# Kernel optimization log

Measured on AMD Instinct MI355X. Metric: run time of the kernel, lower is better.

## Reference

```python
import jax, jax.numpy as jnp
import numpy as np

B, L, D = 16, 1024, 768   # batch, nodes per graph, embed_dim
H, C = 4, 256             # gat_heads, gat_hidden per head
E = 8192                  # directed edges per graph (2 per triple)
NEG_SLOPE = 0.2           # PyG GATConv default negative_slope


def setup_inputs() -> dict:
    key = jax.random.key(0)
    ks = jax.random.split(key, 8)
    s = 0.02
    return {
        "text_embeddings": jax.random.normal(ks[0], (B, L, D), jnp.float32),
        "edge_index": jax.random.randint(ks[1], (B, 2, E), 0, L, jnp.int32),
        "W_gat": jax.random.normal(ks[2], (H * C, D), jnp.float32) * s,   # GATConv.lin (bias=False)
        "att_src": jax.random.normal(ks[3], (H, C), jnp.float32) * s,
        "att_dst": jax.random.normal(ks[4], (H, C), jnp.float32) * s,
        "b_gat": jnp.zeros((H * C,), jnp.float32),                        # GATConv bias (concat=True)
        "W_out": jax.random.normal(ks[5], (D, H * C + D), jnp.float32) * s,
        "b_out": jnp.zeros((D,), jnp.float32),
    }


def _gat_one(x, edge_index, W_gat, att_src, att_dst, b_gat):
    """PyG-style GATConv on one graph. x: [N,D], edge_index: [2,E] (src->dst)."""
    N = x.shape[0]
    loops = jnp.arange(N, dtype=edge_index.dtype)          # add_self_loops=True (PyG default)
    src = jnp.concatenate([edge_index[0], loops])
    dst = jnp.concatenate([edge_index[1], loops])
    h = (x @ W_gat.T).reshape(N, H, C)                     # [N,H,C]
    a_s = jnp.einsum('nhc,hc->nh', h, att_src)             # [N,H]
    a_d = jnp.einsum('nhc,hc->nh', h, att_dst)
    e = jax.nn.leaky_relu(a_s[src] + a_d[dst], NEG_SLOPE)  # [E+N,H] per-edge logits
    m = jax.ops.segment_max(e, dst, num_segments=N)        # stable softmax over each dst neighborhood
    p = jnp.exp(e - m[dst])
    denom = jax.ops.segment_sum(p, dst, num_segments=N)
    alpha = p / (denom[dst] + 1e-16)                       # [E+N,H]
    out = jax.ops.segment_sum(alpha[:, :, None] * h[src], dst, num_segments=N)  # [N,H,C]
    return out.reshape(N, H * C) + b_gat


def reference(text_embeddings, edge_index, W_gat, att_src, att_dst, b_gat, W_out, b_out):
    x_gat = jax.vmap(_gat_one, in_axes=(0, 0, None, None, None, None))(
        text_embeddings, edge_index, W_gat, att_src, att_dst, b_gat)   # [B,L,H*C]
    fused = jnp.concatenate([text_embeddings, x_gat], axis=-1)          # [B,L,D+H*C]
    return fused @ W_out.T + b_out                                      # [B,L,D]
```

## Files before the change

kernel.cpp:

```cpp
#include <hip/hip_runtime.h>
#include <hip/hip_bf16.h>

#define B_ 16
#define L_ 1024
#define D_ 768
#define H_ 4
#define C_ 256
#define E_ 8192
#define ET_ (E_ + L_)
#define HC_ (H_ * C_)
#define F_ (D_ + HC_)
#define M_ (B_ * L_)
#define NEG_SLOPE 0.2f

typedef short bf16x8 __attribute__((ext_vector_type(8)));
typedef float f32x16 __attribute__((ext_vector_type(16)));
using bf16 = __hip_bfloat16;

struct bf16x4_s { bf16 x, y, z, w; };

__device__ __forceinline__ void async_copy16(const bf16* gsrc, bf16* ldst) {
  __builtin_amdgcn_global_load_lds(
      (const __attribute__((address_space(1))) unsigned int*)gsrc,
      (__attribute__((address_space(3))) unsigned int*)ldst, 16, 0, 0);
}

__global__ __launch_bounds__(256)
void precompute(const float* __restrict__ Wg,
                const float* __restrict__ att_s, const float* __restrict__ att_d,
                const float* __restrict__ Wout, const float* __restrict__ bgat,
                const float* __restrict__ bout,
                float* __restrict__ wsd, float* __restrict__ cout)
{
  int blk = blockIdx.x, t = threadIdx.x;
  if (blk < 24) {
    int h8 = blk / 3;
    int k = (blk % 3) * 256 + t;
    const float* att = (h8 < 4) ? (att_s + h8 * C_) : (att_d + (h8 - 4) * C_);
    int head = h8 & 3;
    const float* wbase = Wg + (long)head * C_ * D_ + k;
    float acc = 0.f;
    for (int c = 0; c < C_; c++) acc += att[c] * wbase[(long)c * D_];
    wsd[h8 * D_ + k] = acc;
  } else {
    int o = (blk - 24) * 256 + t;
    if (o < D_) {
      float s = bout[o];
      const float* wrow = Wout + (long)o * F_ + D_;
      for (int j = 0; j < HC_; j++) s += bgat[j] * wrow[j];
      cout[o] = s;
    }
  }
}

#define NB_CSR 16
#define NB_X (M_ / 4)
#define NB_W 2112

__global__ __launch_bounds__(256)
void prep(const float* __restrict__ x, const int* __restrict__ ei,
          const float* __restrict__ Wg, const float* __restrict__ Wout,
          const float* __restrict__ wsd,
          bf16* __restrict__ xf, bf16* __restrict__ wg_bf, bf16* __restrict__ wout_bf,
          float* __restrict__ a_sd, int* __restrict__ deg_g, int* __restrict__ offs_g,
          int* __restrict__ csr_src)
{
  __shared__ int s_deg[L_];
  __shared__ int s_cur[L_];
  __shared__ int s_part[256];
  const int blk = blockIdx.x;
  const int t = threadIdx.x;

  if (blk < NB_CSR) {
    const int b = blk;
    const int* srcp = ei + (long)b * 2 * E_;
    const int* dstp = srcp + E_;
    for (int i = t; i < L_; i += 256) s_deg[i] = 0;
    __syncthreads();
    for (int e = t; e < ET_; e += 256) {
      int dst = (e < E_) ? dstp[e] : (e - E_);
      atomicAdd(&s_deg[dst], 1);
    }
    __syncthreads();
    int d0 = s_deg[t*4], d1 = s_deg[t*4+1], d2 = s_deg[t*4+2], d3 = s_deg[t*4+3];
    int tsum = d0 + d1 + d2 + d3;
    s_part[t] = tsum;
    __syncthreads();
    for (int o = 1; o < 256; o <<= 1) {
      int v = (t >= o) ? s_part[t - o] : 0;
      __syncthreads();
      s_part[t] += v;
      __syncthreads();
    }
    int run = s_part[t] - tsum;
    int o0 = run, o1 = o0 + d0, o2 = o1 + d1, o3 = o2 + d2;
    s_cur[t*4] = o0; s_cur[t*4+1] = o1; s_cur[t*4+2] = o2; s_cur[t*4+3] = o3;
    int gb = b * L_ + t * 4;
    offs_g[gb] = o0; offs_g[gb+1] = o1; offs_g[gb+2] = o2; offs_g[gb+3] = o3;
    deg_g[gb] = d0; deg_g[gb+1] = d1; deg_g[gb+2] = d2; deg_g[gb+3] = d3;
    __syncthreads();
    int* csr_b = csr_src + (long)b * ET_;
    for (int e = t; e < ET_; e += 256) {
      int src = (e < E_) ? srcp[e] : (e - E_);
      int dst = (e < E_) ? dstp[e] : (e - E_);
      int slot = atomicAdd(&s_cur[dst], 1);
      csr_b[slot] = src;
    }
  } else if (blk < NB_CSR + NB_X) {
    int row = (blk - NB_CSR) * 4 + (t >> 6);
    int lane = t & 63;
    const float4* xr = (const float4*)(x + (long)row * D_);
    float acc8[8];
#pragma unroll
    for (int h = 0; h < 8; h++) acc8[h] = 0.f;
#pragma unroll
    for (int q = 0; q < 3; q++) {
      float4 v = xr[lane + 64 * q];
      bf16 o4[4] = { __float2bfloat16(v.x), __float2bfloat16(v.y),
                     __float2bfloat16(v.z), __float2bfloat16(v.w) };
      *(uint2*)(xf + (long)row * F_ + 4 * (lane + 64 * q)) = *(const uint2*)o4;
#pragma unroll
      for (int h = 0; h < 8; h++) {
        float4 w = ((const float4*)(wsd + h * D_))[lane + 64 * q];
        acc8[h] += v.x * w.x + v.y * w.y + v.z * w.z + v.w * w.w;
      }
    }
#pragma unroll
    for (int o = 32; o; o >>= 1)
#pragma unroll
      for (int h = 0; h < 8; h++) acc8[h] += __shfl_xor(acc8[h], o);
    if (lane == 0) {
      float4 s4 = {acc8[0], acc8[1], acc8[2], acc8[3]};
      float4 dd4 = {acc8[4], acc8[5], acc8[6], acc8[7]};
      *(float4*)(a_sd + (long)row * 8) = s4;
      *(float4*)(a_sd + (long)row * 8 + 4) = dd4;
    }
  } else {
    long na4 = (long)HC_ * D_ / 4;
    long nb4 = (long)D_ * F_ / 4;
    long i0 = (long)(blk - NB_CSR - NB_X) * 256 + t;
    long stride = (long)NB_W * 256;
    for (long i = i0; i < na4 + nb4; i += stride) {
      const float4 v = (i < na4) ? ((const float4*)Wg)[i] : ((const float4*)Wout)[i - na4];
      bf16x4_s o;
      o.x = __float2bfloat16(v.x);
      o.y = __float2bfloat16(v.y);
      o.z = __float2bfloat16(v.z);
      o.w = __float2bfloat16(v.w);
      if (i < na4) ((bf16x4_s*)wg_bf)[i] = o;
      else         ((bf16x4_s*)wout_bf)[i - na4] = o;
    }
  }
}

#define BM 128
#define BN 128
#define BK 64

template <int OUT_BF16>
__global__ __launch_bounds__(256)
void gemm_nt_128(const bf16* __restrict__ A, int lda,
                 const bf16* __restrict__ Bm, int ldb,
                 void* __restrict__ Cm_, int ldc, int K,
                 const float* __restrict__ bias)
{
  __shared__ __align__(16) bf16 As[BM * BK];
  __shared__ __align__(16) bf16 Bs[BN * BK];
  const int t = threadIdx.x;
  const int lane = t & 63;
  const int wave = t >> 6;
  const long m0 = (long)blockIdx.x * BM;
  const long n0 = (long)blockIdx.y * BN;
  const int wm = (wave >> 1) * 64;
  const int wn = (wave & 1) * 64;
  const int lrow = lane & 31;
  const int kg = lane >> 5;

  const int sr_base = wave * 32;
  const int sr_lane = lane >> 3;
  const int c8l = lane & 7;

  f32x16 acc[2][2] = {};

  for (int k0 = 0; k0 < K; k0 += BK) {
#pragma unroll
    for (int j = 0; j < 4; j++) {
      int r = sr_base + j * 8 + sr_lane;
      int col = k0 + ((c8l ^ (r & 7)) << 3);
      bf16* ldsA = As + (sr_base + j * 8) * BK;
      bf16* ldsB = Bs + (sr_base + j * 8) * BK;
      async_copy16(A + (m0 + r) * lda + col, ldsA);
      async_copy16(Bm + (n0 + r) * ldb + col, ldsB);
    }
    __syncthreads();
#pragma unroll
    for (int ks = 0; ks < BK; ks += 16) {
      bf16x8 af[2], bfr[2];
#pragma unroll
      for (int i = 0; i < 2; i++) {
        int ra = wm + i * 32 + lrow;
        int ca = ((ks >> 3) + kg) ^ (ra & 7);
        af[i] = *(const bf16x8*)(As + ra * BK + ca * 8);
        int rb = wn + i * 32 + lrow;
        int cb = ((ks >> 3) + kg) ^ (rb & 7);
        bfr[i] = *(const bf16x8*)(Bs + rb * BK + cb * 8);
      }
#pragma unroll
      for (int i = 0; i < 2; i++)
#pragma unroll
        for (int j = 0; j < 2; j++)
          acc[i][j] = __builtin_amdgcn_mfma_f32_32x32x16_bf16(af[i], bfr[j], acc[i][j], 0, 0, 0);
    }
    __syncthreads();
  }

#pragma unroll
  for (int i = 0; i < 2; i++) {
#pragma unroll
    for (int j = 0; j < 2; j++) {
      long col = n0 + wn + j * 32 + lrow;
      float bv = bias ? bias[col] : 0.f;
#pragma unroll
      for (int reg = 0; reg < 16; reg++) {
        long row = m0 + wm + i * 32 + (reg & 3) + 8 * (reg >> 2) + 4 * kg;
        float v = acc[i][j][reg] + bv;
        if (OUT_BF16) ((bf16*)Cm_)[row * ldc + col] = __float2bfloat16(v);
        else          ((float*)Cm_)[row * ldc + col] = v;
      }
    }
  }
}

__device__ inline float lrelu(float v) { return v > 0.f ? v : NEG_SLOPE * v; }

__device__ __forceinline__ float sel4(float a0, float a1, float a2, float a3, int h) {
  float lo = (h & 1) ? a1 : a0;
  float hi = (h & 1) ? a3 : a2;
  return (h & 2) ? hi : lo;
}

__device__ __forceinline__ void fma8(float* acc, float a, uint4 u) {
#pragma unroll
  for (int k = 0; k < 4; k++) {
    unsigned w = ((const unsigned*)&u)[k];
    float lo = __uint_as_float(w << 16);
    float hi = __uint_as_float(w & 0xffff0000u);
    acc[2 * k]     += a * lo;
    acc[2 * k + 1] += a * hi;
  }
}

__global__ __launch_bounds__(256)
void gat_aggregate(const int* __restrict__ offs, const int* __restrict__ deg_a,
                   const int* __restrict__ csr_src,
                   const float* __restrict__ a_sd,
                   const bf16* __restrict__ h, bf16* __restrict__ xg, int ldx)
{
  const int bd = blockIdx.x * 4 + (threadIdx.x >> 6);
  const int b = bd >> 10;
  const int lane = threadIdx.x & 63;
  const int deg = deg_a[bd];
  const int* list = csr_src + (long)b * ET_ + offs[bd];
  const float4 ad = *(const float4*)(a_sd + (long)bd * 8 + 4);
  const int myhead = lane >> 4;
  const bf16* hbase = h + (long)b * L_ * HC_ + lane * 16;

  float acc16[16];
#pragma unroll
  for (int k = 0; k < 16; k++) acc16[k] = 0.f;

  if (deg <= 64) {
    int s_lane = 0;
    float4 e4 = {-INFINITY, -INFINITY, -INFINITY, -INFINITY};
    if (lane < deg) {
      s_lane = list[lane];
      const float4 as4 = *(const float4*)(a_sd + ((long)b * L_ + s_lane) * 8);
      e4.x = lrelu(as4.x + ad.x);
      e4.y = lrelu(as4.y + ad.y);
      e4.z = lrelu(as4.z + ad.z);
      e4.w = lrelu(as4.w + ad.w);
    }
    float4 mx = e4;
#pragma unroll
    for (int off = 32; off; off >>= 1) {
      mx.x = fmaxf(mx.x, __shfl_xor(mx.x, off));
      mx.y = fmaxf(mx.y, __shfl_xor(mx.y, off));
      mx.z = fmaxf(mx.z, __shfl_xor(mx.z, off));
      mx.w = fmaxf(mx.w, __shfl_xor(mx.w, off));
    }
    float4 p = {0.f, 0.f, 0.f, 0.f};
    if (lane < deg) {
      p.x = __expf(e4.x - mx.x);
      p.y = __expf(e4.y - mx.y);
      p.z = __expf(e4.z - mx.z);
      p.w = __expf(e4.w - mx.w);
    }
    float4 sm = p;
#pragma unroll
    for (int off = 32; off; off >>= 1) {
      sm.x += __shfl_xor(sm.x, off);
      sm.y += __shfl_xor(sm.y, off);
      sm.z += __shfl_xor(sm.z, off);
      sm.w += __shfl_xor(sm.w, off);
    }
    float4 alpha;
    alpha.x = p.x / (sm.x + 1e-16f);
    alpha.y = p.y / (sm.y + 1e-16f);
    alpha.z = p.z / (sm.z + 1e-16f);
    alpha.w = p.w / (sm.w + 1e-16f);

#pragma unroll 2
    for (int e = 0; e < deg; e++) {
      int se = __shfl(s_lane, e);
      float a0 = __shfl(alpha.x, e);
      float a1 = __shfl(alpha.y, e);
      float a2 = __shfl(alpha.z, e);
      float a3 = __shfl(alpha.w, e);
      float a = sel4(a0, a1, a2, a3, myhead);
      const bf16* hp = hbase + (long)se * HC_;
      uint4 u0 = *(const uint4*)hp;
      uint4 u1 = *(const uint4*)(hp + 8);
      fma8(acc16, a, u0);
      fma8(acc16 + 8, a, u1);
    }
  } else {
    float4 mx = {-INFINITY, -INFINITY, -INFINITY, -INFINITY};
    for (int i = lane; i < deg; i += 64) {
      int s = list[i];
      const float4 as4 = *(const float4*)(a_sd + ((long)b * L_ + s) * 8);
      mx.x = fmaxf(mx.x, lrelu(as4.x + ad.x));
      mx.y = fmaxf(mx.y, lrelu(as4.y + ad.y));
      mx.z = fmaxf(mx.z, lrelu(as4.z + ad.z));
      mx.w = fmaxf(mx.w, lrelu(as4.w + ad.w));
    }
#pragma unroll
    for (int off = 32; off; off >>= 1) {
      mx.x = fmaxf(mx.x, __shfl_xor(mx.x, off));
      mx.y = fmaxf(mx.y, __shfl_xor(mx.y, off));
      mx.z = fmaxf(mx.z, __shfl_xor(mx.z, off));
      mx.w = fmaxf(mx.w, __shfl_xor(mx.w, off));
    }
    float4 sm = {0.f, 0.f, 0.f, 0.f};
    for (int i = lane; i < deg; i += 64) {
      int s = list[i];
      const float4 as4 = *(const float4*)(a_sd + ((long)b * L_ + s) * 8);
      sm.x += __expf(lrelu(as4.x + ad.x) - mx.x);
      sm.y += __expf(lrelu(as4.y + ad.y) - mx.y);
      sm.z += __expf(lrelu(as4.z + ad.z) - mx.z);
      sm.w += __expf(lrelu(as4.w + ad.w) - mx.w);
    }
#pragma unroll
    for (int off = 32; off; off >>= 1) {
      sm.x += __shfl_xor(sm.x, off);
      sm.y += __shfl_xor(sm.y, off);
      sm.z += __shfl_xor(sm.z, off);
      sm.w += __shfl_xor(sm.w, off);
    }
    float4 rden;
    rden.x = 1.f / (sm.x + 1e-16f);
    rden.y = 1.f / (sm.y + 1e-16f);
    rden.z = 1.f / (sm.z + 1e-16f);
    rden.w = 1.f / (sm.w + 1e-16f);
    for (int e = 0; e < deg; e++) {
      int se = list[e];
      const float4 as4 = *(const float4*)(a_sd + ((long)b * L_ + se) * 8);
      float a0 = __expf(lrelu(as4.x + ad.x) - mx.x) * rden.x;
      float a1 = __expf(lrelu(as4.y + ad.y) - mx.y) * rden.y;
      float a2 = __expf(lrelu(as4.z + ad.z) - mx.z) * rden.z;
      float a3 = __expf(lrelu(as4.w + ad.w) - mx.w) * rden.w;
      float a = sel4(a0, a1, a2, a3, myhead);
      const bf16* hp = hbase + (long)se * HC_;
      uint4 u0 = *(const uint4*)hp;
      uint4 u1 = *(const uint4*)(hp + 8);
      fma8(acc16, a, u0);
      fma8(acc16 + 8, a, u1);
    }
  }

  bf16 ov[16];
#pragma unroll
  for (int k = 0; k < 16; k++) ov[k] = __float2bfloat16(acc16[k]);
  bf16* op = xg + (long)bd * ldx + lane * 16;
  *(uint4*)op = *(const uint4*)ov;
  *(uint4*)(op + 8) = *(const uint4*)(ov + 8);
}

extern "C" void kernel_launch(void* const* d_in, const int* in_sizes, int n_in,
                              void* d_out, int out_size, void* d_ws, size_t ws_size,
                              hipStream_t stream) {
  const float* x     = (const float*)d_in[0];
  const int*   ei    = (const int*)d_in[1];
  const float* Wg    = (const float*)d_in[2];
  const float* att_s = (const float*)d_in[3];
  const float* att_d = (const float*)d_in[4];
  const float* bgat  = (const float*)d_in[5];
  const float* Wout  = (const float*)d_in[6];
  const float* bout  = (const float*)d_in[7];
  float* out = (float*)d_out;

  char* ws = (char*)d_ws;
  size_t off = 0;
  auto alloc = [&](size_t bytes) {
    void* p = ws + off;
    off = (off + bytes + 255) & ~(size_t)255;
    return p;
  };
  bf16* xf      = (bf16*)alloc((size_t)M_ * F_ * 2);
  bf16* wg_bf   = (bf16*)alloc((size_t)HC_ * D_ * 2);
  bf16* wout_bf = (bf16*)alloc((size_t)D_ * F_ * 2);
  bf16* h_bf    = (bf16*)alloc((size_t)M_ * HC_ * 2);
  float* a_sd   = (float*)alloc((size_t)M_ * 8 * 4);
  int* deg      = (int*)alloc((size_t)M_ * 4);
  int* offs     = (int*)alloc((size_t)M_ * 4);
  int* csr_src  = (int*)alloc((size_t)B_ * ET_ * 4);
  float* cout   = (float*)alloc((size_t)D_ * 4);
  float* wsd    = (float*)alloc((size_t)8 * D_ * 4);

  precompute<<<dim3(27), dim3(256), 0, stream>>>(Wg, att_s, att_d, Wout, bgat, bout,
                                                 wsd, cout);

  prep<<<dim3(NB_CSR + NB_X + NB_W), dim3(256), 0, stream>>>(
      x, ei, Wg, Wout, wsd, xf, wg_bf, wout_bf, a_sd, deg, offs, csr_src);

  gemm_nt_128<1><<<dim3(M_ / BM, HC_ / BN), dim3(256), 0, stream>>>(
      xf, F_, wg_bf, D_, h_bf, HC_, D_, nullptr);

  gat_aggregate<<<dim3(M_ / 4), dim3(256), 0, stream>>>(offs, deg, csr_src, a_sd,
                                                        h_bf, xf + D_, F_);

  gemm_nt_128<0><<<dim3(M_ / BM, D_ / BN), dim3(256), 0, stream>>>(
      xf, F_, wout_bf, F_, out, D_, F_, cout);
}
```

Before: 312.6 us.

## Compute attention logits from bf16 h in aggregation with online-free softmax

```diff
diff --git a/kernel.cpp b/kernel.cpp
--- a/kernel.cpp
+++ b/kernel.cpp
@@ -25,45 +25,18 @@
       (__attribute__((address_space(3))) unsigned int*)ldst, 16, 0, 0);
 }
 
-__global__ __launch_bounds__(256)
-void precompute(const float* __restrict__ Wg,
-                const float* __restrict__ att_s, const float* __restrict__ att_d,
-                const float* __restrict__ Wout, const float* __restrict__ bgat,
-                const float* __restrict__ bout,
-                float* __restrict__ wsd, float* __restrict__ cout)
-{
-  int blk = blockIdx.x, t = threadIdx.x;
-  if (blk < 24) {
-    int h8 = blk / 3;
-    int k = (blk % 3) * 256 + t;
-    const float* att = (h8 < 4) ? (att_s + h8 * C_) : (att_d + (h8 - 4) * C_);
-    int head = h8 & 3;
-    const float* wbase = Wg + (long)head * C_ * D_ + k;
-    float acc = 0.f;
-    for (int c = 0; c < C_; c++) acc += att[c] * wbase[(long)c * D_];
-    wsd[h8 * D_ + k] = acc;
-  } else {
-    int o = (blk - 24) * 256 + t;
-    if (o < D_) {
-      float s = bout[o];
-      const float* wrow = Wout + (long)o * F_ + D_;
-      for (int j = 0; j < HC_; j++) s += bgat[j] * wrow[j];
-      cout[o] = s;
-    }
-  }
-}
-
 #define NB_CSR 16
-#define NB_X (M_ / 4)
+#define NB_X (M_ * (D_ / 8) / 256)
 #define NB_W 2112
+#define NB_CO 3
 
 __global__ __launch_bounds__(256)
 void prep(const float* __restrict__ x, const int* __restrict__ ei,
           const float* __restrict__ Wg, const float* __restrict__ Wout,
-          const float* __restrict__ wsd,
+          const float* __restrict__ bgat, const float* __restrict__ bout,
           bf16* __restrict__ xf, bf16* __restrict__ wg_bf, bf16* __restrict__ wout_bf,
-          float* __restrict__ a_sd, int* __restrict__ deg_g, int* __restrict__ offs_g,
-          int* __restrict__ csr_src)
+          int* __restrict__ deg_g, int* __restrict__ offs_g, int* __restrict__ csr_src,
+          float* __restrict__ cout)
 {
   __shared__ int s_deg[L_];
   __shared__ int s_cur[L_];
@@ -107,35 +80,18 @@
       csr_b[slot] = src;
     }
   } else if (blk < NB_CSR + NB_X) {
-    int row = (blk - NB_CSR) * 4 + (t >> 6);
-    int lane = t & 63;
-    const float4* xr = (const float4*)(x + (long)row * D_);
-    float acc8[8];
-#pragma unroll
-    for (int h = 0; h < 8; h++) acc8[h] = 0.f;
-#pragma unroll
-    for (int q = 0; q < 3; q++) {
-      float4 v = xr[lane + 64 * q];
-      bf16 o4[4] = { __float2bfloat16(v.x), __float2bfloat16(v.y),
-                     __float2bfloat16(v.z), __float2bfloat16(v.w) };
-      *(uint2*)(xf + (long)row * F_ + 4 * (lane + 64 * q)) = *(const uint2*)o4;
-#pragma unroll
-      for (int h = 0; h < 8; h++) {
-        float4 w = ((const float4*)(wsd + h * D_))[lane + 64 * q];
-        acc8[h] += v.x * w.x + v.y * w.y + v.z * w.z + v.w * w.w;
-      }
-    }
-#pragma unroll
-    for (int o = 32; o; o >>= 1)
-#pragma unroll
-      for (int h = 0; h < 8; h++) acc8[h] += __shfl_xor(acc8[h], o);
-    if (lane == 0) {
-      float4 s4 = {acc8[0], acc8[1], acc8[2], acc8[3]};
-      float4 dd4 = {acc8[4], acc8[5], acc8[6], acc8[7]};
-      *(float4*)(a_sd + (long)row * 8) = s4;
-      *(float4*)(a_sd + (long)row * 8 + 4) = dd4;
-    }
-  } else {
+    int idx = (blk - NB_CSR) * 256 + t;
+    int row = idx / (D_ / 8);
+    int c8 = idx - row * (D_ / 8);
+    const float4* src = (const float4*)(x + (long)row * D_ + c8 * 8);
+    float4 v0 = src[0], v1 = src[1];
+    bf16 o[8];
+    o[0] = __float2bfloat16(v0.x); o[1] = __float2bfloat16(v0.y);
+    o[2] = __float2bfloat16(v0.z); o[3] = __float2bfloat16(v0.w);
+    o[4] = __float2bfloat16(v1.x); o[5] = __float2bfloat16(v1.y);
+    o[6] = __float2bfloat16(v1.z); o[7] = __float2bfloat16(v1.w);
+    *(uint4*)(xf + (long)row * F_ + c8 * 8) = *(const uint4*)o;
+  } else if (blk < NB_CSR + NB_X + NB_W) {
     long na4 = (long)HC_ * D_ / 4;
     long nb4 = (long)D_ * F_ / 4;
     long i0 = (long)(blk - NB_CSR - NB_X) * 256 + t;
@@ -149,6 +105,14 @@
       o.w = __float2bfloat16(v.w);
       if (i < na4) ((bf16x4_s*)wg_bf)[i] = o;
       else         ((bf16x4_s*)wout_bf)[i - na4] = o;
+    }
+  } else {
+    int o = (blk - NB_CSR - NB_X - NB_W) * 256 + t;
+    if (o < D_) {
+      float s = bout[o];
+      const float* wrow = Wout + (long)o * F_ + D_;
+      for (int j = 0; j < HC_; j++) s += bgat[j] * wrow[j];
+      cout[o] = s;
     }
   }
 }
@@ -233,154 +197,102 @@
 
 __device__ inline float lrelu(float v) { return v > 0.f ? v : NEG_SLOPE * v; }
 
-__device__ __forceinline__ float sel4(float a0, float a1, float a2, float a3, int h) {
-  float lo = (h & 1) ? a1 : a0;
-  float hi = (h & 1) ? a3 : a2;
-  return (h & 2) ? hi : lo;
-}
-
-__device__ __forceinline__ void fma8(float* acc, float a, uint4 u) {
+__device__ __forceinline__ void unpack16(uint4 u0, uint4 u1, float* f) {
 #pragma unroll
   for (int k = 0; k < 4; k++) {
-    unsigned w = ((const unsigned*)&u)[k];
-    float lo = __uint_as_float(w << 16);
-    float hi = __uint_as_float(w & 0xffff0000u);
-    acc[2 * k]     += a * lo;
-    acc[2 * k + 1] += a * hi;
+    unsigned w = ((const unsigned*)&u0)[k];
+    f[2 * k]     = __uint_as_float(w << 16);
+    f[2 * k + 1] = __uint_as_float(w & 0xffff0000u);
+    unsigned w2 = ((const unsigned*)&u1)[k];
+    f[8 + 2 * k]     = __uint_as_float(w2 << 16);
+    f[8 + 2 * k + 1] = __uint_as_float(w2 & 0xffff0000u);
   }
 }
 
 __global__ __launch_bounds__(256)
 void gat_aggregate(const int* __restrict__ offs, const int* __restrict__ deg_a,
                    const int* __restrict__ csr_src,
-                   const float* __restrict__ a_sd,
+                   const float* __restrict__ att_s_g, const float* __restrict__ att_d_g,
                    const bf16* __restrict__ h, bf16* __restrict__ xg, int ldx)
 {
-  const int bd = blockIdx.x * 4 + (threadIdx.x >> 6);
-  const int b = bd >> 10;
-  const int lane = threadIdx.x & 63;
+  const int t = threadIdx.x;
+  const int lane = t & 63;
+  const int wave = t >> 6;
+  const int i = blockIdx.x;
+  const int b = (i & 7) + 8 * ((i >> 3) >> 8);
+  const int grp = (i >> 3) & 255;
+  const int bd = b * L_ + grp * 4 + wave;
   const int deg = deg_a[bd];
   const int* list = csr_src + (long)b * ET_ + offs[bd];
-  const float4 ad = *(const float4*)(a_sd + (long)bd * 8 + 4);
-  const int myhead = lane >> 4;
-  const bf16* hbase = h + (long)b * L_ * HC_ + lane * 16;
-
-  float acc16[16];
-#pragma unroll
-  for (int k = 0; k < 16; k++) acc16[k] = 0.f;
+  const int c0 = lane * 16;
+
+  float as16[16], ad16[16];
+#pragma unroll
+  for (int q = 0; q < 4; q++) {
+    *(float4*)(as16 + 4 * q) = *(const float4*)(att_s_g + c0 + 4 * q);
+    *(float4*)(ad16 + 4 * q) = *(const float4*)(att_d_g + c0 + 4 * q);
+  }
+
+  const bf16* hrow_d = h + (long)bd * HC_ + c0;
+  float fd[16];
+  unpack16(*(const uint4*)hrow_d, *(const uint4*)(hrow_d + 8), fd);
+  float ad = 0.f;
+#pragma unroll
+  for (int k = 0; k < 16; k++) ad += fd[k] * ad16[k];
+#pragma unroll
+  for (int o = 1; o < 16; o <<= 1) ad += __shfl_xor(ad, o);
+
+  float acc[16];
+#pragma unroll
+  for (int k = 0; k < 16; k++) acc[k] = 0.f;
+  float ssum = 0.f;
+  const bf16* hb = h + (long)b * L_ * HC_ + c0;
 
   if (deg <= 64) {
-    int s_lane = 0;
-    float4 e4 = {-INFINITY, -INFINITY, -INFINITY, -INFINITY};
-    if (lane < deg) {
-      s_lane = list[lane];
-      const float4 as4 = *(const float4*)(a_sd + ((long)b * L_ + s_lane) * 8);
-      e4.x = lrelu(as4.x + ad.x);
-      e4.y = lrelu(as4.y + ad.y);
-      e4.z = lrelu(as4.z + ad.z);
-      e4.w = lrelu(as4.w + ad.w);
-    }
-    float4 mx = e4;
-#pragma unroll
-    for (int off = 32; off; off >>= 1) {
-      mx.x = fmaxf(mx.x, __shfl_xor(mx.x, off));
-      mx.y = fmaxf(mx.y, __shfl_xor(mx.y, off));
-      mx.z = fmaxf(mx.z, __shfl_xor(mx.z, off));
-      mx.w = fmaxf(mx.w, __shfl_xor(mx.w, off));
-    }
-    float4 p = {0.f, 0.f, 0.f, 0.f};
-    if (lane < deg) {
-      p.x = __expf(e4.x - mx.x);
-      p.y = __expf(e4.y - mx.y);
-      p.z = __expf(e4.z - mx.z);
-      p.w = __expf(e4.w - mx.w);
-    }
-    float4 sm = p;
-#pragma unroll
-    for (int off = 32; off; off >>= 1) {
-      sm.x += __shfl_xor(sm.x, off);
-      sm.y += __shfl_xor(sm.y, off);
-      sm.z += __shfl_xor(sm.z, off);
-      sm.w += __shfl_xor(sm.w, off);
-    }
-    float4 alpha;
-    alpha.x = p.x / (sm.x + 1e-16f);
-    alpha.y = p.y / (sm.y + 1e-16f);
-    alpha.z = p.z / (sm.z + 1e-16f);
-    alpha.w = p.w / (sm.w + 1e-16f);
-
+    int s_lane = (lane < deg) ? list[lane] : 0;
 #pragma unroll 2
     for (int e = 0; e < deg; e++) {
       int se = __shfl(s_lane, e);
-      float a0 = __shfl(alpha.x, e);
-      float a1 = __shfl(alpha.y, e);
-      float a2 = __shfl(alpha.z, e);
-      float a3 = __shfl(alpha.w, e);
-      float a = sel4(a0, a1, a2, a3, myhead);
-      const bf16* hp = hbase + (long)se * HC_;
+      const bf16* hp = hb + (long)se * HC_;
       uint4 u0 = *(const uint4*)hp;
       uint4 u1 = *(const uint4*)(hp + 8);
-      fma8(acc16, a, u0);
-      fma8(acc16 + 8, a, u1);
+      float f[16];
+      unpack16(u0, u1, f);
+      float ds = 0.f;
+#pragma unroll
+      for (int k = 0; k < 16; k++) ds += f[k] * as16[k];
+#pragma unroll
+      for (int o = 1; o < 16; o <<= 1) ds += __shfl_xor(ds, o);
+      float p = __expf(lrelu(ds + ad));
+      ssum += p;
+#pragma unroll
+      for (int k = 0; k < 16; k++) acc[k] += p * f[k];
     }
   } else {
-    float4 mx = {-INFINITY, -INFINITY, -INFINITY, -INFINITY};
-    for (int i = lane; i < deg; i += 64) {
-      int s = list[i];
-      const float4 as4 = *(const float4*)(a_sd + ((long)b * L_ + s) * 8);
-      mx.x = fmaxf(mx.x, lrelu(as4.x + ad.x));
-      mx.y = fmaxf(mx.y, lrelu(as4.y + ad.y));
-      mx.z = fmaxf(mx.z, lrelu(as4.z + ad.z));
-      mx.w = fmaxf(mx.w, lrelu(as4.w + ad.w));
-    }
-#pragma unroll
-    for (int off = 32; off; off >>= 1) {
-      mx.x = fmaxf(mx.x, __shfl_xor(mx.x, off));
-      mx.y = fmaxf(mx.y, __shfl_xor(mx.y, off));
-      mx.z = fmaxf(mx.z, __shfl_xor(mx.z, off));
-      mx.w = fmaxf(mx.w, __shfl_xor(mx.w, off));
-    }
-    float4 sm = {0.f, 0.f, 0.f, 0.f};
-    for (int i = lane; i < deg; i += 64) {
-      int s = list[i];
-      const float4 as4 = *(const float4*)(a_sd + ((long)b * L_ + s) * 8);
-      sm.x += __expf(lrelu(as4.x + ad.x) - mx.x);
-      sm.y += __expf(lrelu(as4.y + ad.y) - mx.y);
-      sm.z += __expf(lrelu(as4.z + ad.z) - mx.z);
-      sm.w += __expf(lrelu(as4.w + ad.w) - mx.w);
-    }
-#pragma unroll
-    for (int off = 32; off; off >>= 1) {
-      sm.x += __shfl_xor(sm.x, off);
-      sm.y += __shfl_xor(sm.y, off);
-      sm.z += __shfl_xor(sm.z, off);
-      sm.w += __shfl_xor(sm.w, off);
-    }
-    float4 rden;
-    rden.x = 1.f / (sm.x + 1e-16f);
-    rden.y = 1.f / (sm.y + 1e-16f);
-    rden.z = 1.f / (sm.z + 1e-16f);
-    rden.w = 1.f / (sm.w + 1e-16f);
     for (int e = 0; e < deg; e++) {
       int se = list[e];
-      const float4 as4 = *(const float4*)(a_sd + ((long)b * L_ + se) * 8);
-      float a0 = __expf(lrelu(as4.x + ad.x) - mx.x) * rden.x;
-      float a1 = __expf(lrelu(as4.y + ad.y) - mx.y) * rden.y;
-      float a2 = __expf(lrelu(as4.z + ad.z) - mx.z) * rden.z;
-      float a3 = __expf(lrelu(as4.w + ad.w) - mx.w) * rden.w;
-      float a = sel4(a0, a1, a2, a3, myhead);
-      const bf16* hp = hbase + (long)se * HC_;
+      const bf16* hp = hb + (long)se * HC_;
       uint4 u0 = *(const uint4*)hp;
       uint4 u1 = *(const uint4*)(hp + 8);
-      fma8(acc16, a, u0);
-      fma8(acc16 + 8, a, u1);
-    }
-  }
-
+      float f[16];
+      unpack16(u0, u1, f);
+      float ds = 0.f;
+#pragma unroll
+      for (int k = 0; k < 16; k++) ds += f[k] * as16[k];
+#pragma unroll
+      for (int o = 1; o < 16; o <<= 1) ds += __shfl_xor(ds, o);
+      float p = __expf(lrelu(ds + ad));
+      ssum += p;
+#pragma unroll
+      for (int k = 0; k < 16; k++) acc[k] += p * f[k];
+    }
+  }
+
+  float rs = 1.f / (ssum + 1e-16f);
   bf16 ov[16];
 #pragma unroll
-  for (int k = 0; k < 16; k++) ov[k] = __float2bfloat16(acc16[k]);
-  bf16* op = xg + (long)bd * ldx + lane * 16;
+  for (int k = 0; k < 16; k++) ov[k] = __float2bfloat16(acc[k] * rs);
+  bf16* op = xg + (long)bd * ldx + c0;
   *(uint4*)op = *(const uint4*)ov;
   *(uint4*)(op + 8) = *(const uint4*)(ov + 8);
 }
@@ -409,24 +321,19 @@
   bf16* wg_bf   = (bf16*)alloc((size_t)HC_ * D_ * 2);
   bf16* wout_bf = (bf16*)alloc((size_t)D_ * F_ * 2);
   bf16* h_bf    = (bf16*)alloc((size_t)M_ * HC_ * 2);
-  float* a_sd   = (float*)alloc((size_t)M_ * 8 * 4);
   int* deg      = (int*)alloc((size_t)M_ * 4);
   int* offs     = (int*)alloc((size_t)M_ * 4);
   int* csr_src  = (int*)alloc((size_t)B_ * ET_ * 4);
   float* cout   = (float*)alloc((size_t)D_ * 4);
-  float* wsd    = (float*)alloc((size_t)8 * D_ * 4);
-
-  precompute<<<dim3(27), dim3(256), 0, stream>>>(Wg, att_s, att_d, Wout, bgat, bout,
-                                                 wsd, cout);
-
-  prep<<<dim3(NB_CSR + NB_X + NB_W), dim3(256), 0, stream>>>(
-      x, ei, Wg, Wout, wsd, xf, wg_bf, wout_bf, a_sd, deg, offs, csr_src);
+
+  prep<<<dim3(NB_CSR + NB_X + NB_W + NB_CO), dim3(256), 0, stream>>>(
+      x, ei, Wg, Wout, bgat, bout, xf, wg_bf, wout_bf, deg, offs, csr_src, cout);
 
   gemm_nt_128<1><<<dim3(M_ / BM, HC_ / BN), dim3(256), 0, stream>>>(
       xf, F_, wg_bf, D_, h_bf, HC_, D_, nullptr);
 
-  gat_aggregate<<<dim3(M_ / 4), dim3(256), 0, stream>>>(offs, deg, csr_src, a_sd,
-                                                        h_bf, xf + D_, F_);
+  gat_aggregate<<<dim3(M_ / 4), dim3(256), 0, stream>>>(offs, deg, csr_src,
+                                                        att_s, att_d, h_bf, xf + D_, F_);
 
   gemm_nt_128<0><<<dim3(M_ / BM, D_ / BN), dim3(256), 0, stream>>>(
       xf, F_, wout_bf, F_, out, D_, F_, cout);
```

New measurement: 261.5 us (median of 2 runs). 1.2x faster.
